# Performance work log

Hardware: AMD Instinct MI355X
Metric: run time of the kernel (lower is better)

Reference implementation:

```python
import jax, jax.numpy as jnp
import numpy as np

B, T, D_IN, H, D_OUT = 4096, 512, 10, 20, 2


def setup_inputs() -> dict:
    key = jax.random.key(0)
    ks = jax.random.split(key, 12)
    s = 1.0 / np.sqrt(H)  # PyTorch-style uniform bound scale (use normal*s)
    return {
        "x": jax.random.normal(ks[0], (B, T, D_IN), jnp.float32),
        "w_ih0": jax.random.normal(ks[1], (H, D_IN), jnp.float32) * s,
        "w_hh0": jax.random.normal(ks[2], (H, H), jnp.float32) * s,
        "b_ih0": jax.random.normal(ks[3], (H,), jnp.float32) * s,
        "b_hh0": jax.random.normal(ks[4], (H,), jnp.float32) * s,
        "w_ih1": jax.random.normal(ks[5], (H, H), jnp.float32) * s,
        "w_hh1": jax.random.normal(ks[6], (H, H), jnp.float32) * s,
        "b_ih1": jax.random.normal(ks[7], (H,), jnp.float32) * s,
        "b_hh1": jax.random.normal(ks[8], (H,), jnp.float32) * s,
        "fc_w": jax.random.normal(ks[9], (D_OUT, H), jnp.float32) * s,
        "fc_b": jax.random.normal(ks[10], (D_OUT,), jnp.float32) * s,
    }


def _rnn_layer(inp, w_ih, w_hh, b_ih, b_hh):
    # inp: [B, T, Din]. Precompute input projection once (batched GEMM),
    # then scan the sequential recurrence: h_t = tanh(x_t W_ih^T + b_ih + h_{t-1} W_hh^T + b_hh)
    xp = jnp.einsum('btd,hd->bth', inp, w_ih) + (b_ih + b_hh)  # [B, T, H]

    def step(h, xt):
        h = jnp.tanh(xt + h @ w_hh.T)
        return h, h

    h0 = jnp.zeros((inp.shape[0], w_hh.shape[0]), inp.dtype)
    _, hs = jax.lax.scan(step, h0, jnp.swapaxes(xp, 0, 1))  # hs: [T, B, H]
    return jnp.swapaxes(hs, 0, 1)  # [B, T, H]


def reference(x, w_ih0, w_hh0, b_ih0, b_hh0, w_ih1, w_hh1, b_ih1, b_hh1, fc_w, fc_b):
    h1 = _rnn_layer(x, w_ih0, w_hh0, b_ih0, b_hh0)
    h2 = _rnn_layer(h1, w_ih1, w_hh1, b_ih1, b_hh1)
    last = h2[:, -1, :]  # [B, H]
    return last @ fc_w.T + fc_b  # [B, D_OUT]
```

## Files before the change

### kernel.cpp

```cpp
#include <hip/hip_runtime.h>
#include <cstdint>

constexpr int B_   = 4096;
constexpr int T_   = 512;
constexpr int DIN  = 10;
constexpr int H_   = 20;
constexpr int DOUT = 2;

constexpr int SPW = 3;
constexpr int CH  = 2;
constexpr int XV  = CH * DIN / 4;

typedef float v2f __attribute__((ext_vector_type(2)));
typedef float v4f __attribute__((ext_vector_type(4)));

__device__ __forceinline__ v2f pkfma(v2f a, v2f b, v2f c) {
    return __builtin_elementwise_fma(a, b, c);
}
__device__ __forceinline__ v2f lohalf(v4f v) { return __builtin_shufflevector(v, v, 0, 1); }
__device__ __forceinline__ v2f hihalf(v4f v) { return __builtin_shufflevector(v, v, 2, 3); }

__device__ __forceinline__ float fast_tanh(float v) {
    float e = __builtin_amdgcn_exp2f(v * 2.885390082f);
    float r = __builtin_amdgcn_rcpf(e + 1.0f);
    return fmaf(-2.0f, r, 1.0f);
}

extern "C" __global__ void __launch_bounds__(64, 1)
rnn_pk2(const float* __restrict__ x,
        const float* __restrict__ w_ih0, const float* __restrict__ w_hh0,
        const float* __restrict__ b_ih0, const float* __restrict__ b_hh0,
        const float* __restrict__ w_ih1, const float* __restrict__ w_hh1,
        const float* __restrict__ b_ih1, const float* __restrict__ b_hh1,
        const float* __restrict__ fc_w, const float* __restrict__ fc_b,
        float* __restrict__ out)
{
    const int lane = threadIdx.x;
    const int sl   = lane / H_;
    const int i    = lane - sl * H_;
    const int samp = blockIdx.x * SPW + sl;
    const int sc   = (samp < B_) ? samp : (B_ - 1);
    const int slc  = (sl < SPW) ? sl : SPW;

    __shared__ __align__(16) float h1s[SPW + 1][H_];
    __shared__ __align__(16) float h2s[SPW + 1][H_];

    v2f wi0p[DIN / 2];
    {
        const v2f* p = reinterpret_cast<const v2f*>(w_ih0 + i * DIN);
        #pragma unroll
        for (int k = 0; k < DIN / 2; ++k) wi0p[k] = p[k];
    }
    v2f wh0p[H_ / 2], wi1p[H_ / 2], wh1p[H_ / 2];
    {
        const v4f* p0 = reinterpret_cast<const v4f*>(w_hh0 + i * H_);
        const v4f* p1 = reinterpret_cast<const v4f*>(w_ih1 + i * H_);
        const v4f* p2 = reinterpret_cast<const v4f*>(w_hh1 + i * H_);
        #pragma unroll
        for (int k = 0; k < H_ / 4; ++k) {
            v4f a = p0[k]; wh0p[2*k] = lohalf(a); wh0p[2*k+1] = hihalf(a);
            v4f b = p1[k]; wi1p[2*k] = lohalf(b); wi1p[2*k+1] = hihalf(b);
            v4f c = p2[k]; wh1p[2*k] = lohalf(c); wh1p[2*k+1] = hihalf(c);
        }
    }
    const float bias0 = b_ih0[i] + b_hh0[i];
    const float bias1 = b_ih1[i] + b_hh1[i];

    v2f h1p[H_ / 2], h2p[H_ / 2];
    #pragma unroll
    for (int k = 0; k < H_ / 2; ++k) {
        h1p[k] = (v2f){0.f, 0.f};
        h2p[k] = (v2f){0.f, 0.f};
    }

    const v4f* xb = reinterpret_cast<const v4f*>(x + (size_t)sc * (T_ * DIN));

    v4f xv[XV];
    #pragma unroll
    for (int k = 0; k < XV; ++k) xv[k] = xb[k];

    auto getpair = [&](int p) -> v2f {
        v4f v = xv[p >> 1];
        return (p & 1) ? hihalf(v) : lohalf(v);
    };

    auto full_step = [&](float xpm) {
        v2f aE = (v2f){xpm, 0.f}, aO = (v2f){0.f, 0.f};
        #pragma unroll
        for (int k = 0; k < H_ / 2; k += 2) {
            aE = pkfma(h1p[k],     wh0p[k],     aE);
            aO = pkfma(h1p[k + 1], wh0p[k + 1], aO);
        }
        v2f as = aE + aO;
        float h1n = fast_tanh(as.x + as.y);

        h1s[slc][i] = h1n;
        v4f h1r[H_ / 4];
        #pragma unroll
        for (int k = 0; k < H_ / 4; ++k)
            h1r[k] = reinterpret_cast<const v4f*>(&h1s[slc][0])[k];

        v2f bE = (v2f){bias1, 0.f}, bO = (v2f){0.f, 0.f};
        #pragma unroll
        for (int k = 0; k < H_ / 2; k += 2) {
            bE = pkfma(h1p[k],     wi1p[k],     bE);
            bO = pkfma(h1p[k + 1], wi1p[k + 1], bO);
        }
        #pragma unroll
        for (int k = 0; k < H_ / 2; k += 2) {
            bE = pkfma(h2p[k],     wh1p[k],     bE);
            bO = pkfma(h2p[k + 1], wh1p[k + 1], bO);
        }
        v2f bs = bE + bO;
        float h2n = fast_tanh(bs.x + bs.y);

        h2s[slc][i] = h2n;
        v4f h2r[H_ / 4];
        #pragma unroll
        for (int k = 0; k < H_ / 4; ++k)
            h2r[k] = reinterpret_cast<const v4f*>(&h2s[slc][0])[k];

        #pragma unroll
        for (int k = 0; k < H_ / 4; ++k) {
            h1p[2*k] = lohalf(h1r[k]); h1p[2*k+1] = hihalf(h1r[k]);
            h2p[2*k] = lohalf(h2r[k]); h2p[2*k+1] = hihalf(h2r[k]);
        }
    };

    auto consume_xp = [&](float (&xp)[CH]) {
        #pragma unroll
        for (int m = 0; m < CH; ++m) {
            v2f acc = (v2f){bias0, 0.f};
            #pragma unroll
            for (int q = 0; q < DIN / 2; ++q)
                acc = pkfma(getpair(m * (DIN / 2) + q), wi0p[q], acc);
            xp[m] = acc.x + acc.y;
        }
    };

    {
        float xp[CH];
        consume_xp(xp);
        #pragma unroll
        for (int k = 0; k < XV; ++k) xv[k] = xb[(CH * DIN) / 4 + k];

        float h1n = fast_tanh(xp[0]);
        h1s[slc][i] = h1n;
        #pragma unroll
        for (int k = 0; k < H_ / 4; ++k) {
            v4f v = reinterpret_cast<const v4f*>(&h1s[slc][0])[k];
            h1p[2*k] = lohalf(v); h1p[2*k+1] = hihalf(v);
        }

        #pragma unroll
        for (int m = 1; m < CH; ++m) full_step(xp[m]);
    }

    for (int t0 = CH; t0 < T_; t0 += CH) {
        float xp[CH];
        consume_xp(xp);
        {
            const int t0n = (t0 + CH < T_) ? (t0 + CH) : 0;
            #pragma unroll
            for (int k = 0; k < XV; ++k) xv[k] = xb[(t0n * DIN) / 4 + k];
        }
        #pragma unroll
        for (int m = 0; m < CH; ++m) full_step(xp[m]);
    }

    {
        v2f bE = (v2f){bias1, 0.f}, bO = (v2f){0.f, 0.f};
        #pragma unroll
        for (int k = 0; k < H_ / 2; k += 2) {
            bE = pkfma(h1p[k],     wi1p[k],     bE);
            bO = pkfma(h1p[k + 1], wi1p[k + 1], bO);
        }
        #pragma unroll
        for (int k = 0; k < H_ / 2; k += 2) {
            bE = pkfma(h2p[k],     wh1p[k],     bE);
            bO = pkfma(h2p[k + 1], wh1p[k + 1], bO);
        }
        v2f bs = bE + bO;
        float h2n = fast_tanh(bs.x + bs.y);
        h2s[slc][i] = h2n;
        #pragma unroll
        for (int k = 0; k < H_ / 4; ++k) {
            v4f v = reinterpret_cast<const v4f*>(&h2s[slc][0])[k];
            h2p[2*k] = lohalf(v); h2p[2*k+1] = hihalf(v);
        }
    }

    if (sl < SPW && samp < B_ && i < DOUT) {
        const v2f* fw = reinterpret_cast<const v2f*>(fc_w + i * H_);
        v2f acc = (v2f){fc_b[i], 0.f};
        #pragma unroll
        for (int k = 0; k < H_ / 2; ++k) acc = pkfma(h2p[k], fw[k], acc);
        out[samp * DOUT + i] = acc.x + acc.y;
    }
}

extern "C" void kernel_launch(void* const* d_in, const int* in_sizes, int n_in,
                              void* d_out, int out_size, void* d_ws, size_t ws_size,
                              hipStream_t stream) {
    (void)in_sizes; (void)n_in; (void)d_ws; (void)ws_size; (void)out_size;
    const float* x     = (const float*)d_in[0];
    const float* w_ih0 = (const float*)d_in[1];
    const float* w_hh0 = (const float*)d_in[2];
    const float* b_ih0 = (const float*)d_in[3];
    const float* b_hh0 = (const float*)d_in[4];
    const float* w_ih1 = (const float*)d_in[5];
    const float* w_hh1 = (const float*)d_in[6];
    const float* b_ih1 = (const float*)d_in[7];
    const float* b_hh1 = (const float*)d_in[8];
    const float* fc_w  = (const float*)d_in[9];
    const float* fc_b  = (const float*)d_in[10];
    float* out = (float*)d_out;

    const int grid = (B_ + SPW - 1) / SPW;
    hipLaunchKernelGGL(rnn_pk2, dim3(grid), dim3(64), 0, stream,
                       x, w_ih0, w_hh0, b_ih0, b_hh0,
                       w_ih1, w_hh1, b_ih1, b_hh1, fc_w, fc_b, out);
}
```

Baseline: 145.2 us.

## Use fp16 dot2 for recurrent matvecs and merge hidden-state LDS exchange

Converts the recurrent and inter-layer weights and the exchanged hidden states to packed fp16. Each dot product now uses the v_dot2 f32-accumulate instruction, which handles two products per instruction instead of packed fp32 FMA. Both layers' hidden states now go into a single fp16 shared-memory row, so one write/read exchange per step replaces two and the LDS traffic is halved. The cost is reduced precision in the weights and recurrent state over 512 steps, which risks accuracy drift against the fp32 reference.

```diff
diff --git a/kernel.cpp b/kernel.cpp
--- a/kernel.cpp
+++ b/kernel.cpp
@@ -11,14 +11,21 @@
 constexpr int CH  = 2;
 constexpr int XV  = CH * DIN / 4;
 
-typedef float v2f __attribute__((ext_vector_type(2)));
-typedef float v4f __attribute__((ext_vector_type(4)));
+typedef float    v2f __attribute__((ext_vector_type(2)));
+typedef float    v4f __attribute__((ext_vector_type(4)));
+typedef _Float16 h2t __attribute__((ext_vector_type(2)));
 
 __device__ __forceinline__ v2f pkfma(v2f a, v2f b, v2f c) {
     return __builtin_elementwise_fma(a, b, c);
 }
-__device__ __forceinline__ v2f lohalf(v4f v) { return __builtin_shufflevector(v, v, 0, 1); }
-__device__ __forceinline__ v2f hihalf(v4f v) { return __builtin_shufflevector(v, v, 2, 3); }
+
+__device__ __forceinline__ float fdot2(h2t a, h2t b, float c) {
+#if __has_builtin(__builtin_amdgcn_fdot2)
+    return __builtin_amdgcn_fdot2(a, b, c, false);
+#else
+    return fmaf((float)a.x, (float)b.x, fmaf((float)a.y, (float)b.y, c));
+#endif
+}
 
 __device__ __forceinline__ float fast_tanh(float v) {
     float e = __builtin_amdgcn_exp2f(v * 2.885390082f);
@@ -26,8 +33,10 @@
     return fmaf(-2.0f, r, 1.0f);
 }
 
+union V4H { v4f f; h2t h[4]; };
+
 extern "C" __global__ void __launch_bounds__(64, 1)
-rnn_pk2(const float* __restrict__ x,
+rnn_h16(const float* __restrict__ x,
         const float* __restrict__ w_ih0, const float* __restrict__ w_hh0,
         const float* __restrict__ b_ih0, const float* __restrict__ b_hh0,
         const float* __restrict__ w_ih1, const float* __restrict__ w_hh1,
@@ -42,35 +51,40 @@
     const int sc   = (samp < B_) ? samp : (B_ - 1);
     const int slc  = (sl < SPW) ? sl : SPW;
 
-    __shared__ __align__(16) float h1s[SPW + 1][H_];
-    __shared__ __align__(16) float h2s[SPW + 1][H_];
-
-    v2f wi0p[DIN / 2];
-    {
-        const v2f* p = reinterpret_cast<const v2f*>(w_ih0 + i * DIN);
-        #pragma unroll
-        for (int k = 0; k < DIN / 2; ++k) wi0p[k] = p[k];
-    }
-    v2f wh0p[H_ / 2], wi1p[H_ / 2], wh1p[H_ / 2];
+    __shared__ __align__(16) _Float16 hs[SPW + 1][2 * H_];
+
+    h2t wh0h[10], wi1h[10], wh1h[10];
     {
         const v4f* p0 = reinterpret_cast<const v4f*>(w_hh0 + i * H_);
         const v4f* p1 = reinterpret_cast<const v4f*>(w_ih1 + i * H_);
         const v4f* p2 = reinterpret_cast<const v4f*>(w_hh1 + i * H_);
         #pragma unroll
-        for (int k = 0; k < H_ / 4; ++k) {
-            v4f a = p0[k]; wh0p[2*k] = lohalf(a); wh0p[2*k+1] = hihalf(a);
-            v4f b = p1[k]; wi1p[2*k] = lohalf(b); wi1p[2*k+1] = hihalf(b);
-            v4f c = p2[k]; wh1p[2*k] = lohalf(c); wh1p[2*k+1] = hihalf(c);
-        }
+        for (int k = 0; k < 5; ++k) {
+            v4f a = p0[k];
+            wh0h[2*k]   = h2t{(_Float16)a.x, (_Float16)a.y};
+            wh0h[2*k+1] = h2t{(_Float16)a.z, (_Float16)a.w};
+            v4f b = p1[k];
+            wi1h[2*k]   = h2t{(_Float16)b.x, (_Float16)b.y};
+            wi1h[2*k+1] = h2t{(_Float16)b.z, (_Float16)b.w};
+            v4f c = p2[k];
+            wh1h[2*k]   = h2t{(_Float16)c.x, (_Float16)c.y};
+            wh1h[2*k+1] = h2t{(_Float16)c.z, (_Float16)c.w};
+        }
+    }
+    v2f wi0p[DIN / 2];
+    {
+        const v2f* p = reinterpret_cast<const v2f*>(w_ih0 + i * DIN);
+        #pragma unroll
+        for (int k = 0; k < DIN / 2; ++k) wi0p[k] = p[k];
     }
     const float bias0 = b_ih0[i] + b_hh0[i];
     const float bias1 = b_ih1[i] + b_hh1[i];
 
-    v2f h1p[H_ / 2], h2p[H_ / 2];
+    h2t h1h[10], h2h[10];
     #pragma unroll
-    for (int k = 0; k < H_ / 2; ++k) {
-        h1p[k] = (v2f){0.f, 0.f};
-        h2p[k] = (v2f){0.f, 0.f};
+    for (int k = 0; k < 10; ++k) {
+        h1h[k] = h2t{(_Float16)0.f, (_Float16)0.f};
+        h2h[k] = h2t{(_Float16)0.f, (_Float16)0.f};
     }
 
     const v4f* xb = reinterpret_cast<const v4f*>(x + (size_t)sc * (T_ * DIN));
@@ -81,50 +95,7 @@
 
     auto getpair = [&](int p) -> v2f {
         v4f v = xv[p >> 1];
-        return (p & 1) ? hihalf(v) : lohalf(v);
-    };
-
-    auto full_step = [&](float xpm) {
-        v2f aE = (v2f){xpm, 0.f}, aO = (v2f){0.f, 0.f};
-        #pragma unroll
-        for (int k = 0; k < H_ / 2; k += 2) {
-            aE = pkfma(h1p[k],     wh0p[k],     aE);
-            aO = pkfma(h1p[k + 1], wh0p[k + 1], aO);
-        }
-        v2f as = aE + aO;
-        float h1n = fast_tanh(as.x + as.y);
-
-        h1s[slc][i] = h1n;
-        v4f h1r[H_ / 4];
-        #pragma unroll
-        for (int k = 0; k < H_ / 4; ++k)
-            h1r[k] = reinterpret_cast<const v4f*>(&h1s[slc][0])[k];
-
-        v2f bE = (v2f){bias1, 0.f}, bO = (v2f){0.f, 0.f};
-        #pragma unroll
-        for (int k = 0; k < H_ / 2; k += 2) {
-            bE = pkfma(h1p[k],     wi1p[k],     bE);
-            bO = pkfma(h1p[k + 1], wi1p[k + 1], bO);
-        }
-        #pragma unroll
-        for (int k = 0; k < H_ / 2; k += 2) {
-            bE = pkfma(h2p[k],     wh1p[k],     bE);
-            bO = pkfma(h2p[k + 1], wh1p[k + 1], bO);
-        }
-        v2f bs = bE + bO;
-        float h2n = fast_tanh(bs.x + bs.y);
-
-        h2s[slc][i] = h2n;
-        v4f h2r[H_ / 4];
-        #pragma unroll
-        for (int k = 0; k < H_ / 4; ++k)
-            h2r[k] = reinterpret_cast<const v4f*>(&h2s[slc][0])[k];
-
-        #pragma unroll
-        for (int k = 0; k < H_ / 4; ++k) {
-            h1p[2*k] = lohalf(h1r[k]); h1p[2*k+1] = hihalf(h1r[k]);
-            h2p[2*k] = lohalf(h2r[k]); h2p[2*k+1] = hihalf(h2r[k]);
-        }
+        return (p & 1) ? (v2f){v.z, v.w} : (v2f){v.x, v.y};
     };
 
     auto consume_xp = [&](float (&xp)[CH]) {
@@ -138,6 +109,52 @@
         }
     };
 
+    auto row_read = [&]() {
+        V4H r[5];
+        #pragma unroll
+        for (int k = 0; k < 5; ++k)
+            r[k].f = reinterpret_cast<const v4f*>(&hs[slc][0])[k];
+        #pragma unroll
+        for (int k = 0; k < 2; ++k) {
+            h1h[4*k+0] = r[k].h[0]; h1h[4*k+1] = r[k].h[1];
+            h1h[4*k+2] = r[k].h[2]; h1h[4*k+3] = r[k].h[3];
+        }
+        h1h[8] = r[2].h[0]; h1h[9] = r[2].h[1];
+        h2h[0] = r[2].h[2]; h2h[1] = r[2].h[3];
+        #pragma unroll
+        for (int k = 0; k < 2; ++k) {
+            h2h[2+4*k+0] = r[3+k].h[0]; h2h[2+4*k+1] = r[3+k].h[1];
+            h2h[2+4*k+2] = r[3+k].h[2]; h2h[2+4*k+3] = r[3+k].h[3];
+        }
+    };
+
+    auto full_step = [&](float xpm) {
+        float a0 = xpm, a1 = 0.f;
+        #pragma unroll
+        for (int k = 0; k < 5; ++k) {
+            a0 = fdot2(h1h[2*k],   wh0h[2*k],   a0);
+            a1 = fdot2(h1h[2*k+1], wh0h[2*k+1], a1);
+        }
+        float h1n = fast_tanh(a0 + a1);
+
+        float b0 = bias1, b1 = 0.f;
+        #pragma unroll
+        for (int k = 0; k < 5; ++k) {
+            b0 = fdot2(h1h[2*k],   wi1h[2*k],   b0);
+            b1 = fdot2(h1h[2*k+1], wi1h[2*k+1], b1);
+        }
+        #pragma unroll
+        for (int k = 0; k < 5; ++k) {
+            b0 = fdot2(h2h[2*k],   wh1h[2*k],   b0);
+            b1 = fdot2(h2h[2*k+1], wh1h[2*k+1], b1);
+        }
+        float h2n = fast_tanh(b0 + b1);
+
+        hs[slc][i]      = (_Float16)h1n;
+        hs[slc][H_ + i] = (_Float16)h2n;
+        row_read();
+    };
+
     {
         float xp[CH];
         consume_xp(xp);
@@ -145,12 +162,9 @@
         for (int k = 0; k < XV; ++k) xv[k] = xb[(CH * DIN) / 4 + k];
 
         float h1n = fast_tanh(xp[0]);
-        h1s[slc][i] = h1n;
-        #pragma unroll
-        for (int k = 0; k < H_ / 4; ++k) {
-            v4f v = reinterpret_cast<const v4f*>(&h1s[slc][0])[k];
-            h1p[2*k] = lohalf(v); h1p[2*k+1] = hihalf(v);
-        }
+        hs[slc][i]      = (_Float16)h1n;
+        hs[slc][H_ + i] = (_Float16)0.f;
+        row_read();
 
         #pragma unroll
         for (int m = 1; m < CH; ++m) full_step(xp[m]);
@@ -168,34 +182,30 @@
         for (int m = 0; m < CH; ++m) full_step(xp[m]);
     }
 
-    {
-        v2f bE = (v2f){bias1, 0.f}, bO = (v2f){0.f, 0.f};
-        #pragma unroll
-        for (int k = 0; k < H_ / 2; k += 2) {
-            bE = pkfma(h1p[k],     wi1p[k],     bE);
-            bO = pkfma(h1p[k + 1], wi1p[k + 1], bO);
-        }
-        #pragma unroll
-        for (int k = 0; k < H_ / 2; k += 2) {
-            bE = pkfma(h2p[k],     wh1p[k],     bE);
-            bO = pkfma(h2p[k + 1], wh1p[k + 1], bO);
-        }
-        v2f bs = bE + bO;
-        float h2n = fast_tanh(bs.x + bs.y);
-        h2s[slc][i] = h2n;
-        #pragma unroll
-        for (int k = 0; k < H_ / 4; ++k) {
-            v4f v = reinterpret_cast<const v4f*>(&h2s[slc][0])[k];
-            h2p[2*k] = lohalf(v); h2p[2*k+1] = hihalf(v);
-        }
+    float h2fin[H_];
+    {
+        float b0 = bias1, b1 = 0.f;
+        #pragma unroll
+        for (int k = 0; k < 5; ++k) {
+            b0 = fdot2(h1h[2*k],   wi1h[2*k],   b0);
+            b1 = fdot2(h1h[2*k+1], wi1h[2*k+1], b1);
+        }
+        #pragma unroll
+        for (int k = 0; k < 5; ++k) {
+            b0 = fdot2(h2h[2*k],   wh1h[2*k],   b0);
+            b1 = fdot2(h2h[2*k+1], wh1h[2*k+1], b1);
+        }
+        float h2n = fast_tanh(b0 + b1);
+        hs[slc][H_ + i] = (_Float16)h2n;
+        #pragma unroll
+        for (int j = 0; j < H_; ++j) h2fin[j] = (float)hs[slc][H_ + j];
     }
 
     if (sl < SPW && samp < B_ && i < DOUT) {
-        const v2f* fw = reinterpret_cast<const v2f*>(fc_w + i * H_);
-        v2f acc = (v2f){fc_b[i], 0.f};
-        #pragma unroll
-        for (int k = 0; k < H_ / 2; ++k) acc = pkfma(h2p[k], fw[k], acc);
-        out[samp * DOUT + i] = acc.x + acc.y;
+        float acc = fc_b[i];
+        #pragma unroll
+        for (int j = 0; j < H_; ++j) acc = fmaf(h2fin[j], fc_w[i * H_ + j], acc);
+        out[samp * DOUT + i] = acc;
     }
 }
 
@@ -217,7 +227,7 @@
     float* out = (float*)d_out;
 
     const int grid = (B_ + SPW - 1) / SPW;
-    hipLaunchKernelGGL(rnn_pk2, dim3(grid), dim3(64), 0, stream,
+    hipLaunchKernelGGL(rnn_h16, dim3(grid), dim3(64), 0, stream,
                        x, w_ih0, w_hh0, b_ih0, b_hh0,
                        w_ih1, w_hh1, b_ih1, b_hh1, fc_w, fc_b, out);
 }
```

Measured after the change: 136.7 us. 1.06x faster.
